# Kernel optimization log

Hardware: AMD Instinct MI355X
Metric: run time of the kernel (lower is better)

## Reference

```python
import jax, jax.numpy as jnp
import numpy as np

B, S, N1, N2, NS = 2048, 1024, 8192, 16384, 256
EPS = 1e-10

def setup_inputs() -> dict:
    key = jax.random.key(0)
    ks = jax.random.split(key, 12)
    t_in = jax.random.uniform(ks[0], (B,), jnp.float32)
    y_in = jax.random.uniform(ks[1], (B, S), jnp.float32)
    den_gas = jax.random.uniform(ks[2], (B, 1), jnp.float32) * 1e4
    alpha_1st = jax.random.uniform(ks[3], (N1,), jnp.float32)
    gamma_1st = jax.random.uniform(ks[4], (N1,), jnp.float32) * 50.0
    alpha_2nd = jax.random.uniform(ks[5], (N2,), jnp.float32)
    gamma_2nd = jax.random.uniform(ks[6], (N2,), jnp.float32) * 50.0
    r1_1st = jax.random.randint(ks[7], (N1,), 0, S, jnp.int32)
    p_1st = jax.random.randint(ks[8], (N1,), 0, S, jnp.int32)
    r1_2nd = jax.random.randint(ks[9], (N2,), 0, S, jnp.int32)
    r2_2nd = jax.random.randint(ks[10], (N2,), 0, S, jnp.int32)
    p_2nd = jax.random.randint(ks[11], (N2,), 0, S, jnp.int32)
    inds_surf = 512 + jnp.arange(NS, dtype=jnp.int32)  # surface species slots
    inds_mant = 768 + jnp.arange(NS, dtype=jnp.int32)  # mantle species slots
    return dict(t_in=t_in, y_in=y_in, den_gas=den_gas,
                alpha_1st=alpha_1st, gamma_1st=gamma_1st,
                alpha_2nd=alpha_2nd, gamma_2nd=gamma_2nd,
                r1_1st=r1_1st, p_1st=p_1st,
                r1_2nd=r1_2nd, r2_2nd=r2_2nd, p_2nd=p_2nd,
                inds_surf=inds_surf, inds_mant=inds_mant)

def reference(t_in, y_in, den_gas, alpha_1st, gamma_1st, alpha_2nd, gamma_2nd,
              r1_1st, p_1st, r1_2nd, r2_2nd, p_2nd, inds_surf, inds_mant):
    zeros = jnp.zeros_like(y_in)
    # medium parameters (module_med): temperature from t, den_norm from den_gas
    T = 10.0 + 5.0 * jax.nn.sigmoid(t_in)[:, None]            # [B,1]
    # rmod_1st / rmod_2nd: modified-Arrhenius rate coefficients
    rates_1st = alpha_1st[None, :] * jnp.exp(-gamma_1st[None, :] / T)      # [B,N1]
    rates_2nd = (alpha_2nd[None, :] * jnp.sqrt(T / 300.0)
                 * jnp.exp(-gamma_2nd[None, :] / T))                       # [B,N2]
    # reaction fluxes (gather)
    terms_1st = rates_1st * y_in[:, r1_1st]                                 # [B,N1]
    terms_2nd = rates_2nd * y_in[:, r1_2nd] * y_in[:, r2_2nd] * den_gas     # [B,N2]
    # surface gain / loss assemblers (gain-only and loss-only scatters)
    gain = (zeros.at[:, p_1st].add(terms_1st)
                 .at[:, p_2nd].add(terms_2nd))[:, inds_surf]
    loss = (zeros.at[:, r1_1st].add(-terms_1st)
                 .at[:, r1_2nd].add(-terms_2nd)
                 .at[:, r2_2nd].add(-terms_2nd))[:, inds_surf]
    dy_surf_gain = jnp.sum(gain, axis=-1, keepdims=True)    # [B,1] >= 0
    dy_surf_loss = -jnp.sum(loss, axis=-1, keepdims=True)   # [B,1] >= 0
    # rmod_smt: surface<->mantle transfer coefficients (three-phase)
    y_surf_tot = jnp.sum(y_in[:, inds_surf], axis=-1, keepdims=True)
    y_mant_tot = jnp.sum(y_in[:, inds_mant], axis=-1, keepdims=True)
    k_s2m = dy_surf_gain / (y_surf_tot + EPS)  # burial rate per surface species
    k_m2s = dy_surf_loss / (y_mant_tot + EPS)  # excavation rate per mantle species
    terms_s2m = k_s2m * y_in[:, inds_surf]     # [B,NS]
    terms_m2s = k_m2s * y_in[:, inds_mant]     # [B,NS]
    # full RHS: asm_smt + asm_1st + asm_2nd
    dy = (zeros
          .at[:, p_1st].add(terms_1st).at[:, r1_1st].add(-terms_1st)
          .at[:, p_2nd].add(terms_2nd)
          .at[:, r1_2nd].add(-terms_2nd).at[:, r2_2nd].add(-terms_2nd)
          .at[:, inds_surf].add(terms_m2s - terms_s2m)
          .at[:, inds_mant].add(terms_s2m - terms_m2s))
    return dy
```

## Files before the change

kernel.cpp:

```cpp
#include <hip/hip_runtime.h>
#include <hip/hip_fp16.h>

constexpr int kB  = 2048;
constexpr int kS  = 1024;
constexpr int kN1 = 8192;
constexpr int kN2 = 16384;
constexpr int kNTERM = kN1 + kN2;
constexpr int kQT    = kNTERM / 4;
constexpr int kRoles = 2*kN1 + 3*kN2;
constexpr float kEPS = 1e-10f;
constexpr int NT = 256;

constexpr int kPitchE   = 48;
constexpr int kGrpU16   = kPitchE * kS;
constexpr int kEllU16   = 4 * kGrpU16;

constexpr size_t kOffCntQ = 0;
constexpr size_t kOffCur  = 16384;
constexpr size_t kOffSpOf = 32768;
constexpr size_t kOffPsOf = 36864;
constexpr size_t kOffCQP  = 40960;
constexpr size_t kOffEll  = 57344;
constexpr size_t kOffRec  = kOffEll + (size_t)kEllU16 * 2;
constexpr size_t kWsNeed  = kOffRec + (size_t)kNTERM * 16;

__device__ __forceinline__ void role_decode(
    int i, const int* r1_1, const int* p_1, const int* r1_2,
    const int* r2_2, const int* p_2, int& s, int& j, bool& neg)
{
    if (i < kN1)                { j = i;       s = p_1[j];  neg = false; }
    else if (i < 2*kN1)         { j = i - kN1; s = r1_1[j]; neg = true;  }
    else if (i < 2*kN1 + kN2)   { int q = i - 2*kN1;         j = kN1 + q; s = p_2[q];  neg = false; }
    else if (i < 2*kN1 + 2*kN2) { int q = i - 2*kN1 - kN2;   j = kN1 + q; s = r1_2[q]; neg = true; }
    else                        { int q = i - 2*kN1 - 2*kN2; j = kN1 + q; s = r2_2[q]; neg = true; }
}

__global__ __launch_bounds__(NT) void count_fill(
    const float* __restrict__ a1, const float* __restrict__ g1,
    const float* __restrict__ a2, const float* __restrict__ g2,
    const int* __restrict__ r1_1, const int* __restrict__ p_1,
    const int* __restrict__ r1_2, const int* __restrict__ r2_2,
    const int* __restrict__ p_2,
    unsigned* __restrict__ cntQ, float4* __restrict__ rec)
{
    int i = blockIdx.x * NT + threadIdx.x;
    if (i >= kRoles) return;
    int s, j; bool neg;
    role_decode(i, r1_1, p_1, r1_2, r2_2, p_2, s, j, neg);
    atomicAdd(&cntQ[(j / kQT) * kS + s], 1u);
    if (i < kNTERM) {
        float4 r;
        if (i < kN1) { r.x = a1[i]; r.y = -g1[i]; r.z = __int_as_float(r1_1[i]); r.w = 0.f; }
        else { int u = i - kN1; r.x = a2[u]; r.y = -g2[u];
               r.z = __int_as_float(r1_2[u]); r.w = __int_as_float(r2_2[u]); }
        rec[i] = r;
    }
}

__global__ __launch_bounds__(1024) void rank_perm(
    const unsigned* __restrict__ cntQ,
    unsigned* __restrict__ sp_of_pos, unsigned* __restrict__ pos_of_sp,
    unsigned* __restrict__ cntQP, unsigned* __restrict__ curC)
{
    __shared__ unsigned hist[768];
    __shared__ unsigned pref[768];
    __shared__ unsigned cur[768];
    const int tid = threadIdx.x;

    if (tid < 768) { hist[tid] = 0; cur[tid] = 0; }
    unsigned c0 = cntQ[tid], c1 = cntQ[kS + tid],
             c2 = cntQ[2*kS + tid], c3 = cntQ[3*kS + tid];
    unsigned tot = c0 + c1 + c2 + c3;
    unsigned cat = (tid < 512) ? 0u : (tid < 768 ? 1u : 2u);
    unsigned bin = cat * 256 + (tot > 255u ? 255u : tot);
    __syncthreads();
    atomicAdd(&hist[bin], 1u);
    __syncthreads();
    if (tid < 768) pref[tid] = hist[tid];
    __syncthreads();
    for (int off = 1; off < 768; off <<= 1) {
        unsigned t = 0;
        if (tid < 768 && tid >= off) t = pref[tid - off];
        __syncthreads();
        if (tid < 768) pref[tid] += t;
        __syncthreads();
    }
    unsigned off_in = atomicAdd(&cur[bin], 1u);
    unsigned pos = pref[bin] - hist[bin] + off_in;
    pos_of_sp[tid] = pos;
    sp_of_pos[pos] = (unsigned)tid;
    cntQP[pos]          = c0;
    cntQP[kS + pos]     = c1;
    cntQP[2*kS + pos]   = c2;
    cntQP[3*kS + pos]   = c3;
    curC[tid] = 0; curC[kS + tid] = 0; curC[2*kS + tid] = 0; curC[3*kS + tid] = 0;
}

__global__ __launch_bounds__(NT) void ell_fill(
    const int* __restrict__ r1_1, const int* __restrict__ p_1,
    const int* __restrict__ r1_2, const int* __restrict__ r2_2,
    const int* __restrict__ p_2,
    const unsigned* __restrict__ pos_of_sp, const unsigned* __restrict__ cntQP,
    unsigned* __restrict__ curC, unsigned short* __restrict__ ell)
{
    int i = blockIdx.x * NT + threadIdx.x;
    if (i >= kRoles) return;

    if (i < 4 * kS) {
        int q = i >> 10, p = i & (kS - 1);
        int c = (int)cntQP[q * kS + p]; c = c < kPitchE ? c : kPitchE;
        int end = (c + 7) & ~7; end = end < kPitchE ? end : kPitchE;
        unsigned base = (unsigned)(q * kGrpU16) + ((unsigned)c >> 3) * (unsigned)(kS * 8) + (unsigned)p * 8u;
        for (int k = c; k < end; ++k)
            ell[base + (unsigned)(k & 7)] = 0;
    }

    int s, j; bool neg;
    role_decode(i, r1_1, p_1, r1_2, r2_2, p_2, s, j, neg);
    int q = j / kQT;
    unsigned p = pos_of_sp[s];
    unsigned short e = (unsigned short)(((j - q * kQT + 1) << 2) | (neg ? 0x8000u : 0u));
    unsigned k = atomicAdd(&curC[q * kS + p], 1u);
    if (k < (unsigned)kPitchE)
        ell[(unsigned)(q * kGrpU16) + (k >> 3) * (unsigned)(kS * 8) + p * 8u + (k & 7u)] = e;
}

template<bool TRACK>
__device__ __forceinline__ void accum8s(
    uint4 e, const __half2* __restrict__ t2,
    float& r0, float& r1, float& a0, float& a1)
{
    const char* tb = (const char*)t2;
    #pragma unroll
    for (int w = 0; w < 4; ++w) {
        unsigned u = (&e.x)[w];
        #pragma unroll
        for (int hh = 0; hh < 2; ++hh) {
            unsigned h = (hh == 0) ? (u & 0xffffu) : (u >> 16);
            unsigned t = *(const unsigned*)(tb + (h & 0x7fffu));
            unsigned ts = t ^ ((h & 0x8000u) * 0x10001u);
            float2 f = __half22float2(*(const __half2*)&ts);
            r0 += f.x; r1 += f.y;
            if (TRACK) {
                float2 g = __half22float2(*(const __half2*)&t);
                a0 += g.x; a1 += g.y;
            }
        }
    }
}

__global__ __launch_bounds__(NT, 4) void three_phase_gather8(
    const float* __restrict__ t_in, const float* __restrict__ y_in,
    const float* __restrict__ den_gas,
    const unsigned* __restrict__ cntQP, const unsigned short* __restrict__ ell,
    const unsigned* __restrict__ sp_of_pos,
    const float4* __restrict__ rec, float* __restrict__ dy)
{
    __shared__ float2  y2[kS];
    __shared__ __half2 terms2[kQT + 1];
    __shared__ float   red[4][8];

    const int tid = threadIdx.x;
    const int b0  = blockIdx.x * 2;

    {
        const float4* s0 = (const float4*)(y_in + (size_t)b0 * kS);
        const float4* s1 = (const float4*)(y_in + (size_t)(b0 + 1) * kS);
        float4 va = s0[tid], vb = s1[tid];
        y2[4*tid+0] = make_float2(va.x, vb.x);
        y2[4*tid+1] = make_float2(va.y, vb.y);
        y2[4*tid+2] = make_float2(va.z, vb.z);
        y2[4*tid+3] = make_float2(va.w, vb.w);
    }
    if (tid == 0) terms2[0] = __halves2half2(__float2half(0.f), __float2half(0.f));

    unsigned sp[4];
    #pragma unroll
    for (int slot = 0; slot < 4; ++slot) sp[slot] = sp_of_pos[tid + slot * NT];

    float T0 = 10.f + 5.f / (1.f + __expf(-t_in[b0]));
    float T1 = 10.f + 5.f / (1.f + __expf(-t_in[b0 + 1]));
    float i0 = 1.f / T0, i1 = 1.f / T1;
    float c20 = __fsqrt_rn(T0 * (1.f / 300.f)) * den_gas[b0];
    float c21 = __fsqrt_rn(T1 * (1.f / 300.f)) * den_gas[b0 + 1];

    float acc[4][2] = {};
    float ab2[2] = {};

    #pragma unroll
    for (int q = 0; q < 4; ++q) {
        __syncthreads();
        const int base = q * kQT;
        #pragma unroll 2
        for (int it = 0; it < kQT / NT; ++it) {
            int j = base + it * NT + tid;
            float4 r = rec[j];
            float al = r.x, ng = r.y;
            int ra = __float_as_int(r.z), rb = __float_as_int(r.w);
            float t0, t1;
            if (j < kN1) {
                float2 ya = y2[ra];
                t0 = al * __expf(ng * i0) * ya.x;
                t1 = al * __expf(ng * i1) * ya.y;
            } else {
                float2 ya = y2[ra], yb = y2[rb];
                t0 = c20 * al * __expf(ng * i0) * ya.x * yb.x;
                t1 = c21 * al * __expf(ng * i1) * ya.y * yb.y;
            }
            terms2[j - base + 1] = __halves2half2(__float2half(t0), __float2half(t1));
        }
        const unsigned* cq = cntQP + q * kS;
        const uint4* bq = (const uint4*)(ell + q * kGrpU16);
        uint4 pf[4]; int cc[4];
        #pragma unroll
        for (int slot = 0; slot < 4; ++slot) {
            int p = tid + slot * NT;
            int c = (int)cq[p]; cc[slot] = c < kPitchE ? c : kPitchE;
            pf[slot] = bq[p];
        }
        __syncthreads();
        #pragma unroll
        for (int slot = 0; slot < 4; ++slot) {
            int p = tid + slot * NT;
            float s0 = 0.f, s1 = 0.f, r0 = 0.f, r1 = 0.f;
            if (slot == 2) accum8s<true >(pf[slot], terms2, s0, s1, r0, r1);
            else           accum8s<false>(pf[slot], terms2, s0, s1, r0, r1);
            int trips = (cc[slot] + 7) >> 3;
            const uint4* ap = bq + p + kS;
            for (int t = 1; t < trips; ++t) {
                uint4 e = *ap; ap += kS;
                if (slot == 2) accum8s<true >(e, terms2, s0, s1, r0, r1);
                else           accum8s<false>(e, terms2, s0, s1, r0, r1);
            }
            acc[slot][0] += s0; acc[slot][1] += s1;
            if (slot == 2) { ab2[0] += r0; ab2[1] += r1; }
        }
    }

    float gn0 = 0.5f * (ab2[0] + acc[2][0]), ls0 = 0.5f * (ab2[0] - acc[2][0]);
    float gn1 = 0.5f * (ab2[1] + acc[2][1]), ls1 = 0.5f * (ab2[1] - acc[2][1]);

    float ys0 = y2[512 + tid].x, ys1 = y2[512 + tid].y;
    float ym0 = y2[768 + tid].x, ym1 = y2[768 + tid].y;
    float v[8] = {gn0, ls0, ys0, ym0, gn1, ls1, ys1, ym1};
    #pragma unroll
    for (int off = 32; off > 0; off >>= 1) {
        #pragma unroll
        for (int w = 0; w < 8; ++w) v[w] += __shfl_down(v[w], off, 64);
    }
    int wave = tid >> 6;
    if ((tid & 63) == 0) {
        #pragma unroll
        for (int w = 0; w < 8; ++w) red[wave][w] = v[w];
    }
    __syncthreads();
    float tv[8];
    #pragma unroll
    for (int w = 0; w < 8; ++w) tv[w] = red[0][w] + red[1][w] + red[2][w] + red[3][w];

    float ks2m0 = tv[0] / (tv[2] + kEPS), km2s0 = tv[1] / (tv[3] + kEPS);
    float ks2m1 = tv[4] / (tv[6] + kEPS), km2s1 = tv[5] / (tv[7] + kEPS);

    float* o0 = dy + (size_t)b0 * kS;
    float* o1 = o0 + kS;
    o0[sp[0]] = acc[0][0];  o1[sp[0]] = acc[0][1];
    o0[sp[1]] = acc[1][0];  o1[sp[1]] = acc[1][1];
    {
        unsigned s2 = sp[2];
        float2 yss = y2[s2], ymm = y2[s2 + 256];
        o0[s2] = acc[2][0] + km2s0 * ymm.x - ks2m0 * yss.x;
        o1[s2] = acc[2][1] + km2s1 * ymm.y - ks2m1 * yss.y;
    }
    {
        unsigned s3 = sp[3];
        float2 yss = y2[s3 - 256], ymm = y2[s3];
        o0[s3] = acc[3][0] + ks2m0 * yss.x - km2s0 * ymm.x;
        o1[s3] = acc[3][1] + ks2m1 * yss.y - km2s1 * ymm.y;
    }
}

__global__ __launch_bounds__(NT) void three_phase_scatter(
    const float* __restrict__ t_in, const float* __restrict__ y_in,
    const float* __restrict__ den_gas,
    const float* __restrict__ alpha_1st, const float* __restrict__ gamma_1st,
    const float* __restrict__ alpha_2nd, const float* __restrict__ gamma_2nd,
    const int* __restrict__ r1_1st, const int* __restrict__ p_1st,
    const int* __restrict__ r1_2nd, const int* __restrict__ r2_2nd,
    const int* __restrict__ p_2nd, float* __restrict__ dy)
{
    __shared__ float y_row[kS];
    __shared__ float accs[kS];
    __shared__ float tot[4];
    const int tid = threadIdx.x;
    const int b   = blockIdx.x;
    ((float4*)y_row)[tid] = ((const float4*)(y_in + (size_t)b * kS))[tid];
    ((float4*)accs)[tid] = make_float4(0.f, 0.f, 0.f, 0.f);
    if (tid < 4) tot[tid] = 0.f;
    float t = t_in[b];
    float T = 10.f + 5.f / (1.f + __expf(-t));
    float invT = 1.f / T, sqT = __fsqrt_rn(T * (1.f / 300.f)), dg = den_gas[b];
    __syncthreads();
    float gain = 0.f, loss = 0.f;
    for (int j = tid; j < kN1; j += NT) {
        int r1 = r1_1st[j], p = p_1st[j];
        float term = alpha_1st[j] * __expf(-gamma_1st[j] * invT) * y_row[r1];
        atomicAdd(&accs[p], term); atomicAdd(&accs[r1], -term);
        if ((unsigned)(p - 512) < 256u) gain += term;
        if ((unsigned)(r1 - 512) < 256u) loss += term;
    }
    for (int j = tid; j < kN2; j += NT) {
        int r1 = r1_2nd[j], r2 = r2_2nd[j], p = p_2nd[j];
        float term = sqT * dg * alpha_2nd[j] * __expf(-gamma_2nd[j] * invT) * y_row[r1] * y_row[r2];
        atomicAdd(&accs[p], term); atomicAdd(&accs[r1], -term); atomicAdd(&accs[r2], -term);
        if ((unsigned)(p - 512) < 256u) gain += term;
        if ((unsigned)(r1 - 512) < 256u) loss += term;
        if ((unsigned)(r2 - 512) < 256u) loss += term;
    }
    float g = gain, l = loss;
    #pragma unroll
    for (int off = 32; off > 0; off >>= 1) { g += __shfl_down(g, off, 64); l += __shfl_down(l, off, 64); }
    if ((tid & 63) == 0) { atomicAdd(&tot[0], g); atomicAdd(&tot[1], l); }
    __syncthreads();
    if (tid < 64) {
        float a2v = 0.f;
        for (int u = tid; u < 256; u += 64) a2v += y_row[512 + u];
        #pragma unroll
        for (int off = 32; off > 0; off >>= 1) a2v += __shfl_down(a2v, off, 64);
        if (tid == 0) tot[2] = a2v;
    } else if (tid < 128) {
        float m2 = 0.f;
        for (int u = tid - 64; u < 256; u += 64) m2 += y_row[768 + u];
        #pragma unroll
        for (int off = 32; off > 0; off >>= 1) m2 += __shfl_down(m2, off, 64);
        if (tid == 64) tot[3] = m2;
    }
    __syncthreads();
    float k_s2m = tot[0] / (tot[2] + kEPS);
    float k_m2s = tot[1] / (tot[3] + kEPS);
    float* out = dy + (size_t)b * kS;
    for (int s = tid; s < kS; s += NT) {
        float v = accs[s];
        if ((unsigned)(s - 512) < 256u) v += k_m2s * y_row[s + 256] - k_s2m * y_row[s];
        else if (s >= 768)              v += k_s2m * y_row[s - 256] - k_m2s * y_row[s];
        out[s] = v;
    }
}

extern "C" void kernel_launch(void* const* d_in, const int* in_sizes, int n_in,
                              void* d_out, int out_size, void* d_ws, size_t ws_size,
                              hipStream_t stream) {
    const float* t_in      = (const float*)d_in[0];
    const float* y_in      = (const float*)d_in[1];
    const float* den_gas   = (const float*)d_in[2];
    const float* alpha_1st = (const float*)d_in[3];
    const float* gamma_1st = (const float*)d_in[4];
    const float* alpha_2nd = (const float*)d_in[5];
    const float* gamma_2nd = (const float*)d_in[6];
    const int*   r1_1st    = (const int*)d_in[7];
    const int*   p_1st     = (const int*)d_in[8];
    const int*   r1_2nd    = (const int*)d_in[9];
    const int*   r2_2nd    = (const int*)d_in[10];
    const int*   p_2nd     = (const int*)d_in[11];
    float* dy = (float*)d_out;

    if (ws_size >= kWsNeed) {
        char* ws = (char*)d_ws;
        unsigned*       cntQ      = (unsigned*)(ws + kOffCntQ);
        unsigned*       curC      = (unsigned*)(ws + kOffCur);
        unsigned*       sp_of_pos = (unsigned*)(ws + kOffSpOf);
        unsigned*       pos_of_sp = (unsigned*)(ws + kOffPsOf);
        unsigned*       cntQP     = (unsigned*)(ws + kOffCQP);
        unsigned short* ell       = (unsigned short*)(ws + kOffEll);
        float4*         rec       = (float4*)(ws + kOffRec);
        hipMemsetAsync(cntQ, 0, 16384, stream);
        count_fill<<<kRoles / NT, NT, 0, stream>>>(
            alpha_1st, gamma_1st, alpha_2nd, gamma_2nd,
            r1_1st, p_1st, r1_2nd, r2_2nd, p_2nd, cntQ, rec);
        rank_perm<<<1, 1024, 0, stream>>>(cntQ, sp_of_pos, pos_of_sp, cntQP, curC);
        ell_fill<<<kRoles / NT, NT, 0, stream>>>(
            r1_1st, p_1st, r1_2nd, r2_2nd, p_2nd,
            pos_of_sp, cntQP, curC, ell);
        three_phase_gather8<<<kB / 2, NT, 0, stream>>>(
            t_in, y_in, den_gas, cntQP, ell, sp_of_pos, rec, dy);
    } else {
        three_phase_scatter<<<kB, NT, 0, stream>>>(
            t_in, y_in, den_gas, alpha_1st, gamma_1st, alpha_2nd, gamma_2nd,
            r1_1st, p_1st, r1_2nd, r2_2nd, p_2nd, dy);
    }
}
```

Before: 163.5 us.

## Fuse index-build kernels into one cooperative launch; accumulate gathers in half2

```diff
diff --git a/kernel.cpp b/kernel.cpp
--- a/kernel.cpp
+++ b/kernel.cpp
@@ -1,5 +1,8 @@
 #include <hip/hip_runtime.h>
 #include <hip/hip_fp16.h>
+#include <hip/hip_cooperative_groups.h>
+
+namespace cg = cooperative_groups;
 
 constexpr int kB  = 2048;
 constexpr int kS  = 1024;
@@ -33,6 +36,90 @@
     else if (i < 2*kN1 + kN2)   { int q = i - 2*kN1;         j = kN1 + q; s = p_2[q];  neg = false; }
     else if (i < 2*kN1 + 2*kN2) { int q = i - 2*kN1 - kN2;   j = kN1 + q; s = r1_2[q]; neg = true; }
     else                        { int q = i - 2*kN1 - 2*kN2; j = kN1 + q; s = r2_2[q]; neg = true; }
+}
+
+__global__ __launch_bounds__(1024) void coop_build(
+    const float* __restrict__ a1, const float* __restrict__ g1,
+    const float* __restrict__ a2, const float* __restrict__ g2,
+    const int* __restrict__ r1_1, const int* __restrict__ p_1,
+    const int* __restrict__ r1_2, const int* __restrict__ r2_2,
+    const int* __restrict__ p_2,
+    unsigned* __restrict__ cntQ, unsigned* __restrict__ curC,
+    unsigned* __restrict__ sp_of_pos, unsigned* __restrict__ pos_of_sp,
+    unsigned* __restrict__ cntQP, unsigned short* __restrict__ ell,
+    float4* __restrict__ rec)
+{
+    cg::grid_group grid = cg::this_grid();
+    __shared__ unsigned hist[768];
+    __shared__ unsigned pref[768];
+    __shared__ unsigned cur[768];
+
+    const int tid = threadIdx.x;
+    const int gid = blockIdx.x * 1024 + tid;
+
+    if (gid < 4 * kS) { cntQ[gid] = 0; curC[gid] = 0; }
+    grid.sync();
+
+    int s, j; bool neg;
+    role_decode(gid, r1_1, p_1, r1_2, r2_2, p_2, s, j, neg);
+    int q = j / kQT;
+    atomicAdd(&cntQ[q * kS + s], 1u);
+    if (gid < kNTERM) {
+        float4 r;
+        if (gid < kN1) { r.x = a1[gid]; r.y = -g1[gid];
+                         r.z = __int_as_float(r1_1[gid]); r.w = 0.f; }
+        else { int u = gid - kN1; r.x = a2[u]; r.y = -g2[u];
+               r.z = __int_as_float(r1_2[u]); r.w = __int_as_float(r2_2[u]); }
+        rec[gid] = r;
+    }
+    grid.sync();
+
+    if (blockIdx.x == 0) {
+        if (tid < 768) { hist[tid] = 0; cur[tid] = 0; }
+        unsigned c0 = cntQ[tid], c1 = cntQ[kS + tid],
+                 c2 = cntQ[2*kS + tid], c3 = cntQ[3*kS + tid];
+        unsigned tot = c0 + c1 + c2 + c3;
+        unsigned cat = (tid < 512) ? 0u : (tid < 768 ? 1u : 2u);
+        unsigned bin = cat * 256 + (tot > 255u ? 255u : tot);
+        __syncthreads();
+        atomicAdd(&hist[bin], 1u);
+        __syncthreads();
+        if (tid < 768) pref[tid] = hist[tid];
+        __syncthreads();
+        for (int off = 1; off < 768; off <<= 1) {
+            unsigned t = 0;
+            if (tid < 768 && tid >= off) t = pref[tid - off];
+            __syncthreads();
+            if (tid < 768) pref[tid] += t;
+            __syncthreads();
+        }
+        unsigned off_in = atomicAdd(&cur[bin], 1u);
+        unsigned pos = pref[bin] - hist[bin] + off_in;
+        pos_of_sp[tid] = pos;
+        sp_of_pos[pos] = (unsigned)tid;
+        cntQP[pos]        = c0;
+        cntQP[kS + pos]   = c1;
+        cntQP[2*kS + pos] = c2;
+        cntQP[3*kS + pos] = c3;
+    }
+    grid.sync();
+
+    if (gid < 4 * kS) {
+        int qq = gid >> 10, p = gid & (kS - 1);
+        int c = (int)cntQP[qq * kS + p]; c = c < kPitchE ? c : kPitchE;
+        int end = (c + 7) & ~7; end = end < kPitchE ? end : kPitchE;
+        unsigned base = (unsigned)(qq * kGrpU16)
+                      + ((unsigned)c >> 3) * (unsigned)(kS * 8) + (unsigned)p * 8u;
+        for (int k = c; k < end; ++k)
+            ell[base + (unsigned)(k & 7)] = 0;
+    }
+    {
+        unsigned p = pos_of_sp[s];
+        unsigned short e = (unsigned short)(((j - q * kQT + 1) << 2) | (neg ? 0x8000u : 0u));
+        unsigned k = atomicAdd(&curC[q * kS + p], 1u);
+        if (k < (unsigned)kPitchE)
+            ell[(unsigned)(q * kGrpU16) + (k >> 3) * (unsigned)(kS * 8) + p * 8u + (k & 7u)] = e;
+    }
 }
 
 __global__ __launch_bounds__(NT) void count_fill(
@@ -66,7 +153,6 @@
     __shared__ unsigned pref[768];
     __shared__ unsigned cur[768];
     const int tid = threadIdx.x;
-
     if (tid < 768) { hist[tid] = 0; cur[tid] = 0; }
     unsigned c0 = cntQ[tid], c1 = cntQ[kS + tid],
              c2 = cntQ[2*kS + tid], c3 = cntQ[3*kS + tid];
@@ -89,10 +175,10 @@
     unsigned pos = pref[bin] - hist[bin] + off_in;
     pos_of_sp[tid] = pos;
     sp_of_pos[pos] = (unsigned)tid;
-    cntQP[pos]          = c0;
-    cntQP[kS + pos]     = c1;
-    cntQP[2*kS + pos]   = c2;
-    cntQP[3*kS + pos]   = c3;
+    cntQP[pos]        = c0;
+    cntQP[kS + pos]   = c1;
+    cntQP[2*kS + pos] = c2;
+    cntQP[3*kS + pos] = c3;
     curC[tid] = 0; curC[kS + tid] = 0; curC[2*kS + tid] = 0; curC[3*kS + tid] = 0;
 }
 
@@ -105,16 +191,15 @@
 {
     int i = blockIdx.x * NT + threadIdx.x;
     if (i >= kRoles) return;
-
     if (i < 4 * kS) {
         int q = i >> 10, p = i & (kS - 1);
         int c = (int)cntQP[q * kS + p]; c = c < kPitchE ? c : kPitchE;
         int end = (c + 7) & ~7; end = end < kPitchE ? end : kPitchE;
-        unsigned base = (unsigned)(q * kGrpU16) + ((unsigned)c >> 3) * (unsigned)(kS * 8) + (unsigned)p * 8u;
+        unsigned base = (unsigned)(q * kGrpU16)
+                      + ((unsigned)c >> 3) * (unsigned)(kS * 8) + (unsigned)p * 8u;
         for (int k = c; k < end; ++k)
             ell[base + (unsigned)(k & 7)] = 0;
     }
-
     int s, j; bool neg;
     role_decode(i, r1_1, p_1, r1_2, r2_2, p_2, s, j, neg);
     int q = j / kQT;
@@ -126,11 +211,13 @@
 }
 
 template<bool TRACK>
-__device__ __forceinline__ void accum8s(
+__device__ __forceinline__ void accum8h(
     uint4 e, const __half2* __restrict__ t2,
     float& r0, float& r1, float& a0, float& a1)
 {
     const char* tb = (const char*)t2;
+    __half2 sacc = __halves2half2(__float2half(0.f), __float2half(0.f));
+    __half2 racc = sacc;
     #pragma unroll
     for (int w = 0; w < 4; ++w) {
         unsigned u = (&e.x)[w];
@@ -139,17 +226,16 @@
             unsigned h = (hh == 0) ? (u & 0xffffu) : (u >> 16);
             unsigned t = *(const unsigned*)(tb + (h & 0x7fffu));
             unsigned ts = t ^ ((h & 0x8000u) * 0x10001u);
-            float2 f = __half22float2(*(const __half2*)&ts);
-            r0 += f.x; r1 += f.y;
-            if (TRACK) {
-                float2 g = __half22float2(*(const __half2*)&t);
-                a0 += g.x; a1 += g.y;
-            }
+            sacc = __hadd2(sacc, *(const __half2*)&ts);
+            if (TRACK) racc = __hadd2(racc, *(const __half2*)&t);
         }
     }
-}
-
-__global__ __launch_bounds__(NT, 4) void three_phase_gather8(
+    float2 f = __half22float2(sacc);
+    r0 += f.x; r1 += f.y;
+    if (TRACK) { float2 g = __half22float2(racc); a0 += g.x; a1 += g.y; }
+}
+
+__global__ __launch_bounds__(NT, 4) void three_phase_gather9(
     const float* __restrict__ t_in, const float* __restrict__ y_in,
     const float* __restrict__ den_gas,
     const unsigned* __restrict__ cntQP, const unsigned short* __restrict__ ell,
@@ -223,14 +309,14 @@
         for (int slot = 0; slot < 4; ++slot) {
             int p = tid + slot * NT;
             float s0 = 0.f, s1 = 0.f, r0 = 0.f, r1 = 0.f;
-            if (slot == 2) accum8s<true >(pf[slot], terms2, s0, s1, r0, r1);
-            else           accum8s<false>(pf[slot], terms2, s0, s1, r0, r1);
+            if (slot == 2) accum8h<true >(pf[slot], terms2, s0, s1, r0, r1);
+            else           accum8h<false>(pf[slot], terms2, s0, s1, r0, r1);
             int trips = (cc[slot] + 7) >> 3;
             const uint4* ap = bq + p + kS;
             for (int t = 1; t < trips; ++t) {
                 uint4 e = *ap; ap += kS;
-                if (slot == 2) accum8s<true >(e, terms2, s0, s1, r0, r1);
-                else           accum8s<false>(e, terms2, s0, s1, r0, r1);
+                if (slot == 2) accum8h<true >(e, terms2, s0, s1, r0, r1);
+                else           accum8h<false>(e, terms2, s0, s1, r0, r1);
             }
             acc[slot][0] += s0; acc[slot][1] += s1;
             if (slot == 2) { ab2[0] += r0; ab2[1] += r1; }
@@ -276,73 +362,6 @@
         float2 yss = y2[s3 - 256], ymm = y2[s3];
         o0[s3] = acc[3][0] + ks2m0 * yss.x - km2s0 * ymm.x;
         o1[s3] = acc[3][1] + ks2m1 * yss.y - km2s1 * ymm.y;
-    }
-}
-
-__global__ __launch_bounds__(NT) void three_phase_scatter(
-    const float* __restrict__ t_in, const float* __restrict__ y_in,
-    const float* __restrict__ den_gas,
-    const float* __restrict__ alpha_1st, const float* __restrict__ gamma_1st,
-    const float* __restrict__ alpha_2nd, const float* __restrict__ gamma_2nd,
-    const int* __restrict__ r1_1st, const int* __restrict__ p_1st,
-    const int* __restrict__ r1_2nd, const int* __restrict__ r2_2nd,
-    const int* __restrict__ p_2nd, float* __restrict__ dy)
-{
-    __shared__ float y_row[kS];
-    __shared__ float accs[kS];
-    __shared__ float tot[4];
-    const int tid = threadIdx.x;
-    const int b   = blockIdx.x;
-    ((float4*)y_row)[tid] = ((const float4*)(y_in + (size_t)b * kS))[tid];
-    ((float4*)accs)[tid] = make_float4(0.f, 0.f, 0.f, 0.f);
-    if (tid < 4) tot[tid] = 0.f;
-    float t = t_in[b];
-    float T = 10.f + 5.f / (1.f + __expf(-t));
-    float invT = 1.f / T, sqT = __fsqrt_rn(T * (1.f / 300.f)), dg = den_gas[b];
-    __syncthreads();
-    float gain = 0.f, loss = 0.f;
-    for (int j = tid; j < kN1; j += NT) {
-        int r1 = r1_1st[j], p = p_1st[j];
-        float term = alpha_1st[j] * __expf(-gamma_1st[j] * invT) * y_row[r1];
-        atomicAdd(&accs[p], term); atomicAdd(&accs[r1], -term);
-        if ((unsigned)(p - 512) < 256u) gain += term;
-        if ((unsigned)(r1 - 512) < 256u) loss += term;
-    }
-    for (int j = tid; j < kN2; j += NT) {
-        int r1 = r1_2nd[j], r2 = r2_2nd[j], p = p_2nd[j];
-        float term = sqT * dg * alpha_2nd[j] * __expf(-gamma_2nd[j] * invT) * y_row[r1] * y_row[r2];
-        atomicAdd(&accs[p], term); atomicAdd(&accs[r1], -term); atomicAdd(&accs[r2], -term);
-        if ((unsigned)(p - 512) < 256u) gain += term;
-        if ((unsigned)(r1 - 512) < 256u) loss += term;
-        if ((unsigned)(r2 - 512) < 256u) loss += term;
-    }
-    float g = gain, l = loss;
-    #pragma unroll
-    for (int off = 32; off > 0; off >>= 1) { g += __shfl_down(g, off, 64); l += __shfl_down(l, off, 64); }
-    if ((tid & 63) == 0) { atomicAdd(&tot[0], g); atomicAdd(&tot[1], l); }
-    __syncthreads();
-    if (tid < 64) {
-        float a2v = 0.f;
-        for (int u = tid; u < 256; u += 64) a2v += y_row[512 + u];
-        #pragma unroll
-        for (int off = 32; off > 0; off >>= 1) a2v += __shfl_down(a2v, off, 64);
-        if (tid == 0) tot[2] = a2v;
-    } else if (tid < 128) {
-        float m2 = 0.f;
-        for (int u = tid - 64; u < 256; u += 64) m2 += y_row[768 + u];
-        #pragma unroll
-        for (int off = 32; off > 0; off >>= 1) m2 += __shfl_down(m2, off, 64);
-        if (tid == 64) tot[3] = m2;
-    }
-    __syncthreads();
-    float k_s2m = tot[0] / (tot[2] + kEPS);
-    float k_m2s = tot[1] / (tot[3] + kEPS);
-    float* out = dy + (size_t)b * kS;
-    for (int s = tid; s < kS; s += NT) {
-        float v = accs[s];
-        if ((unsigned)(s - 512) < 256u) v += k_m2s * y_row[s + 256] - k_s2m * y_row[s];
-        else if (s >= 768)              v += k_s2m * y_row[s - 256] - k_m2s * y_row[s];
-        out[s] = v;
     }
 }
 
@@ -363,15 +382,24 @@
     const int*   p_2nd     = (const int*)d_in[11];
     float* dy = (float*)d_out;
 
-    if (ws_size >= kWsNeed) {
-        char* ws = (char*)d_ws;
-        unsigned*       cntQ      = (unsigned*)(ws + kOffCntQ);
-        unsigned*       curC      = (unsigned*)(ws + kOffCur);
-        unsigned*       sp_of_pos = (unsigned*)(ws + kOffSpOf);
-        unsigned*       pos_of_sp = (unsigned*)(ws + kOffPsOf);
-        unsigned*       cntQP     = (unsigned*)(ws + kOffCQP);
-        unsigned short* ell       = (unsigned short*)(ws + kOffEll);
-        float4*         rec       = (float4*)(ws + kOffRec);
+    char* ws = (char*)d_ws;
+    unsigned*       cntQ      = (unsigned*)(ws + kOffCntQ);
+    unsigned*       curC      = (unsigned*)(ws + kOffCur);
+    unsigned*       sp_of_pos = (unsigned*)(ws + kOffSpOf);
+    unsigned*       pos_of_sp = (unsigned*)(ws + kOffPsOf);
+    unsigned*       cntQP     = (unsigned*)(ws + kOffCQP);
+    unsigned short* ell       = (unsigned short*)(ws + kOffEll);
+    float4*         rec       = (float4*)(ws + kOffRec);
+
+    void* cargs[] = {
+        (void*)&alpha_1st, (void*)&gamma_1st, (void*)&alpha_2nd, (void*)&gamma_2nd,
+        (void*)&r1_1st, (void*)&p_1st, (void*)&r1_2nd, (void*)&r2_2nd, (void*)&p_2nd,
+        (void*)&cntQ, (void*)&curC, (void*)&sp_of_pos, (void*)&pos_of_sp,
+        (void*)&cntQP, (void*)&ell, (void*)&rec
+    };
+    hipError_t cerr = hipLaunchCooperativeKernel(
+        (const void*)coop_build, dim3(kRoles / 1024), dim3(1024), cargs, 0, stream);
+    if (cerr != hipSuccess) {
         hipMemsetAsync(cntQ, 0, 16384, stream);
         count_fill<<<kRoles / NT, NT, 0, stream>>>(
             alpha_1st, gamma_1st, alpha_2nd, gamma_2nd,
@@ -380,11 +408,7 @@
         ell_fill<<<kRoles / NT, NT, 0, stream>>>(
             r1_1st, p_1st, r1_2nd, r2_2nd, p_2nd,
             pos_of_sp, cntQP, curC, ell);
-        three_phase_gather8<<<kB / 2, NT, 0, stream>>>(
-            t_in, y_in, den_gas, cntQP, ell, sp_of_pos, rec, dy);
-    } else {
-        three_phase_scatter<<<kB, NT, 0, stream>>>(
-            t_in, y_in, den_gas, alpha_1st, gamma_1st, alpha_2nd, gamma_2nd,
-            r1_1st, p_1st, r1_2nd, r2_2nd, p_2nd, dy);
-    }
-}
+    }
+    three_phase_gather9<<<kB / 2, NT, 0, stream>>>(
+        t_in, y_in, den_gas, cntQP, ell, sp_of_pos, rec, dy);
+}
```

Measured after the change: 211.1 us. 1.29x slower.
